# Kernel tuning notes

Measured on AMD Instinct MI355X. Metric: run time of the kernel, lower is better.

## Reference

```python
import jax, jax.numpy as jnp
import numpy as np

B, T, D = 8, 2048, 128        # batch, time, input_dim
C, CD = 8192, 128             # codebook_size, codebook_dim
COMMIT_W = 1.0                # commitment_weight
IN2Q_W = 0.25                 # input_to_quantize_commit_loss_weight
EPS = 1e-12


def setup_inputs() -> dict:
    key = jax.random.key(0)
    k = jax.random.split(key, 4)
    z = jax.random.normal(k[0], (B, T, D), jnp.float32)
    frozen_codebook = jax.random.normal(k[1], (C, CD), jnp.float32) * CD ** -0.5
    conv_v = jax.random.normal(k[2], (D, CD), jnp.float32) * CD ** -0.5  # weight-norm direction (1x1 conv weight squeezed)
    conv_g = jnp.linalg.norm(conv_v, axis=1)                             # weight-norm gain (torch init: g = ||v||)
    conv_b = jnp.zeros((D,), jnp.float32)
    return {"z": z, "frozen_codebook": frozen_codebook, "conv_v": conv_v,
            "conv_g": conv_g, "conv_b": conv_b}


def _implicit_codebook(fc, v, g, b):
    # weight-normed 1x1 conv == linear: w = g * v / ||v||_row ; out = fc @ w.T + b
    w = g[:, None] * v / jnp.linalg.norm(v, axis=1, keepdims=True)
    return fc @ w.T + b  # (C, D)


def _rotate_to(src, tgt):
    # rotation trick (Fifty et al.): Householder-style rotation, grads flow only through src
    sg = jax.lax.stop_gradient
    norm_src = jnp.linalg.norm(src, axis=-1, keepdims=True)
    norm_tgt = jnp.linalg.norm(tgt, axis=-1, keepdims=True)
    u = sg(src / jnp.maximum(norm_src, EPS))
    q = sg(tgt / jnp.maximum(norm_tgt, EPS))
    w = u + q
    w = sg(w / jnp.maximum(jnp.linalg.norm(w, axis=-1, keepdims=True), EPS))
    e = src
    rotated = (e
               - 2.0 * jnp.sum(e * w, -1, keepdims=True) * w
               + 2.0 * jnp.sum(e * u, -1, keepdims=True) * q)
    scale = sg(norm_tgt / jnp.maximum(norm_src, EPS))
    return rotated * scale


def reference(z, frozen_codebook, conv_v, conv_g, conv_b):
    sg = jax.lax.stop_gradient
    cb = _implicit_codebook(frozen_codebook, conv_v, conv_g, conv_b)  # (C, D)
    # squared euclidean distances -> same argmin as torch.cdist (p=2)
    d2 = (jnp.sum(z * z, -1, keepdims=True)
          - 2.0 * jnp.einsum('btd,cd->btc', z, cb)
          + jnp.sum(cb * cb, -1))                                     # (B, T, C)
    indices = jnp.argmin(d2, axis=-1)                                 # (B, T)
    z_q = cb[indices]                                                 # (B, T, D)
    commit = (jnp.mean((sg(z) - z_q) ** 2)
              + IN2Q_W * jnp.mean((z - sg(z_q)) ** 2))
    z_q = _rotate_to(z, z_q)
    return z_q, indices, commit * COMMIT_W
```

## Files before the change

kernel.cpp:

```cpp
#include <hip/hip_runtime.h>
#include <math.h>

#define NROWS 16384
#define DIM 128
#define NCODE 8192
#define EPSF 1e-12f

typedef float f32x4 __attribute__((ext_vector_type(4)));
typedef __bf16 bf16x8 __attribute__((ext_vector_type(8)));
typedef unsigned short u16x8 __attribute__((ext_vector_type(8)));

#define WS_NEED_BYTES 31571968ull

#define KT 12
#define TILEA 4096
#define TILEB 8192

__device__ __forceinline__ float wave_sum(float x) {
#pragma unroll
  for (int off = 32; off > 0; off >>= 1) x += __shfl_xor(x, off, 64);
  return x;
}

__device__ __forceinline__ unsigned short f2bf(float x) {
  union { float f; unsigned int u; } v;
  v.f = x;
  unsigned int r = v.u + 0x7fffu + ((v.u >> 16) & 1u);
  return (unsigned short)(r >> 16);
}
__device__ __forceinline__ float bf2f(unsigned short h) {
  union { float f; unsigned int u; } v;
  v.u = ((unsigned int)h) << 16;
  return v.f;
}

__device__ __forceinline__ void gload_lds16(const unsigned short* g,
                                            unsigned short* l) {
  __builtin_amdgcn_global_load_lds(
      (const __attribute__((address_space(1))) void*)g,
      (__attribute__((address_space(3))) void*)l, 16, 0, 0);
}

__global__ void wprep_kernel(const float* __restrict__ v,
                             const float* __restrict__ g,
                             float* __restrict__ Wt) {
  const int d = blockIdx.x;
  const int lane = threadIdx.x;
  const float v0 = v[d * DIM + lane], v1 = v[d * DIM + lane + 64];
  const float ss = wave_sum(fmaf(v0, v0, v1 * v1));
  const float sc = g[d] / sqrtf(ss);
  Wt[lane * DIM + d] = v0 * sc;
  Wt[(lane + 64) * DIM + d] = v1 * sc;
}

__global__ __launch_bounds__(256, 2) void codebook_kernel(
    const float* __restrict__ fc, const float* __restrict__ Wt,
    const float* __restrict__ bias, float* __restrict__ cb,
    float* __restrict__ cnorm2, unsigned short* __restrict__ cbcat) {
  __shared__ float Ws[DIM][DIM];
  const int tid = threadIdx.x;
  for (int i = tid; i < 4096; i += 256)
    *(float4*)&Ws[0][i << 2] = *(const float4*)&Wt[i << 2];
  __syncthreads();

  const int lane = tid & 63, wid = tid >> 6;
  const int c0 = blockIdx.x * 16 + wid * 4;
  const float b0 = bias[lane], b1 = bias[lane + 64];

  for (int cc = 0; cc < 4; ++cc) {
    const int c = __builtin_amdgcn_readfirstlane(c0 + cc);
    float a0 = 0.f, a1 = 0.f;
    for (int k = 0; k < DIM; k += 4) {
      const float4 f4 = *(const float4*)&fc[c * DIM + k];
      a0 = fmaf(f4.x, Ws[k][lane], a0);
      a1 = fmaf(f4.x, Ws[k][lane + 64], a1);
      a0 = fmaf(f4.y, Ws[k + 1][lane], a0);
      a1 = fmaf(f4.y, Ws[k + 1][lane + 64], a1);
      a0 = fmaf(f4.z, Ws[k + 2][lane], a0);
      a1 = fmaf(f4.z, Ws[k + 2][lane + 64], a1);
      a0 = fmaf(f4.w, Ws[k + 3][lane], a0);
      a1 = fmaf(f4.w, Ws[k + 3][lane + 64], a1);
    }
    const float o0 = a0 + b0, o1 = a1 + b1;
    cb[c * DIM + lane] = o0;
    cb[c * DIM + lane + 64] = o1;
    const float ss = wave_sum(fmaf(o0, o0, o1 * o1));
    if (lane == 0) cnorm2[c] = ss;

    if (cbcat != nullptr) {
      const int ct = c >> 8, r = c & 255;
      const unsigned int swz = ((r >> 1) & 3) << 3;
      unsigned short* base = cbcat + (size_t)ct * (KT * TILEB);
#pragma unroll
      for (int h = 0; h < 2; ++h) {
        const int d = lane + 64 * h;
        const float val = h ? o1 : o0;
        const unsigned short hi = f2bf(val);
        const unsigned short lo = f2bf(val - bf2f(hi));
        const int ktl = d >> 5;
        const int off = (r << 5) + ((d & 31) ^ swz);
        base[ktl * TILEB + off] = hi;
        base[(4 + ktl) * TILEB + off] = lo;
        base[(8 + ktl) * TILEB + off] = hi;
      }
    }
  }
}

__global__ __launch_bounds__(256) void zprep_kernel(
    const float* __restrict__ z, unsigned short* __restrict__ zcat) {
  const int id = blockIdx.x * 256 + threadIdx.x;
  const int row = id / 48, s = id - row * 48;
  const int kt = s >> 2, s4 = s & 3;
  const int seg = kt >> 2;
  const int d0 = ((kt & 3) << 5) + (s4 << 3);
  const int r = row & 127, rt = row >> 7;
  const int slotsw = s4 ^ ((r >> 1) & 3);

  const float* zp = &z[(size_t)row * DIM + d0];
  u16x8 out;
#pragma unroll
  for (int i = 0; i < 8; ++i) {
    const float x = zp[i];
    unsigned short b = f2bf(x);
    if (seg == 2) b = f2bf(x - bf2f(b));
    out[i] = b;
  }
  *(u16x8*)&zcat[(size_t)(rt * KT + kt) * TILEA + (r << 5) + (slotsw << 3)] =
      out;
}

__global__ __launch_bounds__(512, 4) void mfma_argmin_kernel(
    const unsigned short* __restrict__ zcat,
    const unsigned short* __restrict__ cbcat,
    const float* __restrict__ cnorm2, float* __restrict__ pval,
    int* __restrict__ pidx) {
  __shared__ __align__(16) unsigned short S[TILEA + TILEB];

  const int xcd = blockIdx.x & 7, idx = blockIdx.x >> 3;
  const int rt = xcd * 16 + (idx & 15);
  const int ct = idx >> 4;

  const int tid = threadIdx.x;
  const int lane = tid & 63, wid = tid >> 6;
  const int wr = wid >> 2, wc = wid & 3;
  const int l15 = lane & 15, lg = lane >> 4;
  const int tid8 = tid * 8;

  const unsigned short* Ag = zcat + (size_t)rt * (KT * TILEA);
  const unsigned short* Bg = cbcat + (size_t)ct * (KT * TILEB);

  f32x4 acc[4][4];
#pragma unroll
  for (int mi = 0; mi < 4; ++mi)
#pragma unroll
    for (int ni = 0; ni < 4; ++ni) acc[mi][ni] = f32x4{0.f, 0.f, 0.f, 0.f};

  int aoff[4], boff[4];
#pragma unroll
  for (int i = 0; i < 4; ++i) {
    const int ra = wr * 64 + i * 16 + l15;
    aoff[i] = (ra << 5) + ((lg ^ ((ra >> 1) & 3)) << 3);
    const int rc = wc * 64 + i * 16 + l15;
    boff[i] = TILEA + (rc << 5) + ((lg ^ ((rc >> 1) & 3)) << 3);
  }

  for (int kt = 0; kt < KT; ++kt) {
    __syncthreads();
    gload_lds16(Ag + kt * TILEA + tid8, &S[tid8]);
    gload_lds16(Bg + kt * TILEB + tid8, &S[TILEA + tid8]);
    gload_lds16(Bg + kt * TILEB + 4096 + tid8, &S[TILEA + 4096 + tid8]);
    __syncthreads();

    bf16x8 af[4], bfr[4];
#pragma unroll
    for (int i = 0; i < 4; ++i) af[i] = *(const bf16x8*)&S[aoff[i]];
#pragma unroll
    for (int i = 0; i < 4; ++i) bfr[i] = *(const bf16x8*)&S[boff[i]];
#pragma unroll
    for (int mi = 0; mi < 4; ++mi)
#pragma unroll
      for (int ni = 0; ni < 4; ++ni)
        acc[mi][ni] = __builtin_amdgcn_mfma_f32_16x16x32_bf16(
            af[mi], bfr[ni], acc[mi][ni], 0, 0, 0);
  }
  __syncthreads();

  float* exv = (float*)&S[0];
  int* exi = (int*)&S[2048];

  float cn[4];
#pragma unroll
  for (int ni = 0; ni < 4; ++ni)
    cn[ni] = cnorm2[ct * 256 + wc * 64 + ni * 16 + l15];

#pragma unroll
  for (int mi = 0; mi < 4; ++mi) {
#pragma unroll
    for (int rg = 0; rg < 4; ++rg) {
      float bv = 3.4e38f;
      int bi = 0;
#pragma unroll
      for (int ni = 0; ni < 4; ++ni) {
        const float d = fmaf(-2.f, acc[mi][ni][rg], cn[ni]);
        if (d < bv) { bv = d; bi = ct * 256 + wc * 64 + ni * 16 + l15; }
      }
#pragma unroll
      for (int off = 1; off < 16; off <<= 1) {
        const float ov = __shfl_xor(bv, off, 64);
        const int oi = __shfl_xor(bi, off, 64);
        if (ov < bv || (ov == bv && oi < bi)) { bv = ov; bi = oi; }
      }
      if (l15 == 0) {
        const int rloc = wr * 64 + mi * 16 + (lg << 2) + rg;
        exv[wc * 128 + rloc] = bv;
        exi[wc * 128 + rloc] = bi;
      }
    }
  }
  __syncthreads();
  if (tid < 128) {
    float bv = exv[tid];
    int bi = exi[tid];
#pragma unroll
    for (int w = 1; w < 4; ++w) {
      const float v = exv[w * 128 + tid];
      if (v < bv) { bv = v; bi = exi[w * 128 + tid]; }
    }
    const int row = rt * 128 + tid;
    pval[(size_t)ct * NROWS + row] = bv;
    pidx[(size_t)ct * NROWS + row] = bi;
  }
}

__global__ __launch_bounds__(256, 1) void argmin_kernel(
    const float* __restrict__ z, const float* __restrict__ cb,
    const float* __restrict__ cnorm2, float* __restrict__ pval,
    int* __restrict__ pidx) {
  __shared__ float zs[128][DIM];
  __shared__ float cs[128][DIM];

  const int tid = threadIdx.x;
  const int rb = blockIdx.x >> 1;
  const int ch = blockIdx.x & 1;
  const int row0 = rb * 128;
  const int code0 = ch * (NCODE / 2);

  for (int i = tid; i < 128 * 32; i += 256) {
    const int r = i >> 5, f = i & 31;
    *(float4*)&zs[r][f << 2] = *(const float4*)&z[(row0 + r) * DIM + (f << 2)];
  }

  const int tx = tid & 15, ty = tid >> 4;
  const int sw = tx & 7;

  float best[8];
  int besti[8];
#pragma unroll
  for (int r = 0; r < 8; ++r) { best[r] = 3.4e38f; besti[r] = 0; }

  for (int cc = 0; cc < NCODE / 2; cc += 128) {
    __syncthreads();
    for (int i = tid; i < 128 * 32; i += 256) {
      const int r = i >> 5, f = i & 31;
      const int fg = f ^ (r & 7);
      *(float4*)&cs[r][f << 2] =
          *(const float4*)&cb[(code0 + cc + r) * DIM + (fg << 2)];
    }
    __syncthreads();

    float acc[8][8];
#pragma unroll
    for (int r = 0; r < 8; ++r)
#pragma unroll
      for (int j = 0; j < 8; ++j) acc[r][j] = 0.f;

    for (int k = 0; k < DIM; k += 4) {
      const int f = k >> 2;
      float4 zr[8], cr[8];
#pragma unroll
      for (int r = 0; r < 8; ++r) zr[r] = *(const float4*)&zs[ty + 16 * r][k];
      const int col = ((f ^ sw) << 2);
#pragma unroll
      for (int j = 0; j < 8; ++j) cr[j] = *(const float4*)&cs[tx + 16 * j][col];
#pragma unroll
      for (int r = 0; r < 8; ++r)
#pragma unroll
        for (int j = 0; j < 8; ++j) {
          acc[r][j] = fmaf(zr[r].x, cr[j].x, acc[r][j]);
          acc[r][j] = fmaf(zr[r].y, cr[j].y, acc[r][j]);
          acc[r][j] = fmaf(zr[r].z, cr[j].z, acc[r][j]);
          acc[r][j] = fmaf(zr[r].w, cr[j].w, acc[r][j]);
        }
    }

#pragma unroll
    for (int j = 0; j < 8; ++j) {
      const int code = code0 + cc + tx + 16 * j;
      const float cnv = cnorm2[code];
#pragma unroll
      for (int r = 0; r < 8; ++r) {
        const float s = fmaf(-2.f, acc[r][j], cnv);
        if (s < best[r]) { best[r] = s; besti[r] = code; }
      }
    }
  }

#pragma unroll
  for (int off = 1; off < 16; off <<= 1) {
#pragma unroll
    for (int r = 0; r < 8; ++r) {
      const float ov = __shfl_xor(best[r], off, 64);
      const int oi = __shfl_xor(besti[r], off, 64);
      if (ov < best[r] || (ov == best[r] && oi < besti[r])) {
        best[r] = ov;
        besti[r] = oi;
      }
    }
  }
  if (tx == 0) {
#pragma unroll
    for (int r = 0; r < 8; ++r) {
      const int row = row0 + ty + 16 * r;
      pval[(size_t)ch * NROWS + row] = best[r];
      pidx[(size_t)ch * NROWS + row] = besti[r];
    }
  }
}

__global__ __launch_bounds__(256) void rotate_kernel(
    const float* __restrict__ z, const float* __restrict__ cb,
    const float* __restrict__ pval, const int* __restrict__ pidx, int ntiles,
    float* __restrict__ out_zq, float* __restrict__ out_idx,
    float* __restrict__ partials) {
  const int tid = threadIdx.x;
  const int wid = tid >> 6, lane = tid & 63;
  const int row = blockIdx.x * 4 + wid;

  float bv = 3.4e38f;
  int bi = 0x7fffffff;
  if (lane < ntiles) {
    bv = pval[(size_t)lane * NROWS + row];
    bi = pidx[(size_t)lane * NROWS + row];
  }
#pragma unroll
  for (int off = 32; off > 0; off >>= 1) {
    const float ov = __shfl_xor(bv, off, 64);
    const int oi = __shfl_xor(bi, off, 64);
    if (ov < bv || (ov == bv && oi < bi)) { bv = ov; bi = oi; }
  }
  const int ci = bi;

  const float z0 = z[row * DIM + lane], z1 = z[row * DIM + lane + 64];
  const float c0 = cb[ci * DIM + lane], c1 = cb[ci * DIM + lane + 64];

  const float ns2 = wave_sum(fmaf(z0, z0, z1 * z1));
  const float nt2 = wave_sum(fmaf(c0, c0, c1 * c1));
  const float ns = sqrtf(ns2), nt = sqrtf(nt2);
  const float dns = fmaxf(ns, EPSF), dnt = fmaxf(nt, EPSF);
  const float u0 = z0 / dns, u1 = z1 / dns;
  const float q0 = c0 / dnt, q1 = c1 / dnt;
  float w0 = u0 + q0, w1 = u1 + q1;
  const float nw = sqrtf(wave_sum(fmaf(w0, w0, w1 * w1)));
  const float dnw = fmaxf(nw, EPSF);
  w0 /= dnw;
  w1 /= dnw;
  const float ew = wave_sum(fmaf(z0, w0, z1 * w1));
  const float eu = wave_sum(fmaf(z0, u0, z1 * u1));
  const float sc = nt / dns;
  const float o0 = (z0 - 2.f * ew * w0 + 2.f * eu * q0) * sc;
  const float o1 = (z1 - 2.f * ew * w1 + 2.f * eu * q1) * sc;
  out_zq[row * DIM + lane] = o0;
  out_zq[row * DIM + lane + 64] = o1;
  if (lane == 0) out_idx[row] = (float)ci;

  const float d0 = z0 - c0, d1 = z1 - c1;
  const float rsum = wave_sum(fmaf(d0, d0, d1 * d1));
  __shared__ float pr[4];
  if (lane == 0) pr[wid] = rsum;
  __syncthreads();
  if (tid == 0) partials[blockIdx.x] = (pr[0] + pr[1]) + (pr[2] + pr[3]);
}

__global__ void finalize_kernel(const float* __restrict__ partials,
                                float* __restrict__ out_commit) {
  __shared__ float red[256];
  const int tid = threadIdx.x;
  float s = 0.f;
  for (int i = tid; i < 4096; i += 256) s += partials[i];
  red[tid] = s;
  __syncthreads();
  for (int off = 128; off > 0; off >>= 1) {
    if (tid < off) red[tid] += red[tid + off];
    __syncthreads();
  }
  if (tid == 0) out_commit[0] = red[0] * (1.25f / ((float)NROWS * (float)DIM));
}

extern "C" void kernel_launch(void* const* d_in, const int* in_sizes, int n_in,
                              void* d_out, int out_size, void* d_ws,
                              size_t ws_size, hipStream_t stream) {
  const float* z = (const float*)d_in[0];
  const float* fc = (const float*)d_in[1];
  const float* conv_v = (const float*)d_in[2];
  const float* conv_g = (const float*)d_in[3];
  const float* conv_b = (const float*)d_in[4];
  float* out = (float*)d_out;

  float* ws = (float*)d_ws;
  float* cb = ws;
  float* cnorm2 = ws + 1048576;
  float* Wt = ws + 1056768;

  if (ws_size >= WS_NEED_BYTES) {
    unsigned short* zcat = (unsigned short*)(ws + 1073152);
    unsigned short* cbcat = (unsigned short*)(ws + 4218880);
    float* pval = ws + 5791744;
    int* pidx = (int*)(ws + 6840320);
    float* partials = ws + 7888896;

    wprep_kernel<<<DIM, 64, 0, stream>>>(conv_v, conv_g, Wt);
    codebook_kernel<<<NCODE / 16, 256, 0, stream>>>(fc, Wt, conv_b, cb, cnorm2,
                                                    cbcat);
    zprep_kernel<<<NROWS * 48 / 256, 256, 0, stream>>>(z, zcat);
    mfma_argmin_kernel<<<4096, 512, 0, stream>>>(zcat, cbcat, cnorm2, pval,
                                                 pidx);
    rotate_kernel<<<NROWS / 4, 256, 0, stream>>>(z, cb, pval, pidx, 32, out,
                                                 out + 2097152, partials);
    finalize_kernel<<<1, 256, 0, stream>>>(partials, out + 2113536);
  } else {
    float* pval = ws + 1073152;
    int* pidx = (int*)(ws + 1105920);
    float* partials = ws + 1138688;

    wprep_kernel<<<DIM, 64, 0, stream>>>(conv_v, conv_g, Wt);
    codebook_kernel<<<NCODE / 16, 256, 0, stream>>>(fc, Wt, conv_b, cb, cnorm2,
                                                    nullptr);
    argmin_kernel<<<256, 256, 0, stream>>>(z, cb, cnorm2, pval, pidx);
    rotate_kernel<<<NROWS / 4, 256, 0, stream>>>(z, cb, pval, pidx, 2, out,
                                                 out + 2097152, partials);
    finalize_kernel<<<1, 256, 0, stream>>>(partials, out + 2113536);
  }
}
```

Before: 212.8 us.

## Double-buffer LDS tiles to overlap global loads with MFMA compute

Splits the shared-memory staging buffer into two halves and prefetches the next K tile with direct global-to-LDS loads while MFMAs consume the current one. Manual vmcnt waits and raw s_barrier calls replace the two __syncthreads per iteration, and the K loop is fully unrolled. This is meant to hide global load latency in the distance GEMM. In exchange LDS use doubles to about 48KB per block, which may limit occupancy under launch_bounds(512,4).

```diff
diff --git a/kernel.cpp b/kernel.cpp
--- a/kernel.cpp
+++ b/kernel.cpp
@@ -15,6 +15,7 @@
 #define KT 12
 #define TILEA 4096
 #define TILEB 8192
+#define CHUNK (TILEA + TILEB)
 
 __device__ __forceinline__ float wave_sum(float x) {
 #pragma unroll
@@ -95,13 +96,13 @@
       for (int h = 0; h < 2; ++h) {
         const int d = lane + 64 * h;
         const float val = h ? o1 : o0;
-        const unsigned short hi = f2bf(val);
-        const unsigned short lo = f2bf(val - bf2f(hi));
+        const unsigned short hiv = f2bf(val);
+        const unsigned short lov = f2bf(val - bf2f(hiv));
         const int ktl = d >> 5;
         const int off = (r << 5) + ((d & 31) ^ swz);
-        base[ktl * TILEB + off] = hi;
-        base[(4 + ktl) * TILEB + off] = lo;
-        base[(8 + ktl) * TILEB + off] = hi;
+        base[ktl * TILEB + off] = hiv;
+        base[(4 + ktl) * TILEB + off] = lov;
+        base[(8 + ktl) * TILEB + off] = hiv;
       }
     }
   }
@@ -135,7 +136,7 @@
     const unsigned short* __restrict__ cbcat,
     const float* __restrict__ cnorm2, float* __restrict__ pval,
     int* __restrict__ pidx) {
-  __shared__ __align__(16) unsigned short S[TILEA + TILEB];
+  __shared__ __align__(16) unsigned short S[2 * CHUNK];
 
   const int xcd = blockIdx.x & 7, idx = blockIdx.x >> 3;
   const int rt = xcd * 16 + (idx & 15);
@@ -150,6 +151,14 @@
   const unsigned short* Ag = zcat + (size_t)rt * (KT * TILEA);
   const unsigned short* Bg = cbcat + (size_t)ct * (KT * TILEB);
 
+#define STAGE(ktile, buf)                                                  \
+  do {                                                                     \
+    gload_lds16(Ag + (ktile)*TILEA + tid8, &S[(buf)*CHUNK + tid8]);        \
+    gload_lds16(Bg + (ktile)*TILEB + tid8, &S[(buf)*CHUNK + TILEA + tid8]); \
+    gload_lds16(Bg + (ktile)*TILEB + 4096 + tid8,                          \
+                &S[(buf)*CHUNK + TILEA + 4096 + tid8]);                    \
+  } while (0)
+
   f32x4 acc[4][4];
 #pragma unroll
   for (int mi = 0; mi < 4; ++mi)
@@ -165,25 +174,38 @@
     boff[i] = TILEA + (rc << 5) + ((lg ^ ((rc >> 1) & 3)) << 3);
   }
 
+  STAGE(0, 0);
+
+#pragma unroll
   for (int kt = 0; kt < KT; ++kt) {
-    __syncthreads();
-    gload_lds16(Ag + kt * TILEA + tid8, &S[tid8]);
-    gload_lds16(Bg + kt * TILEB + tid8, &S[TILEA + tid8]);
-    gload_lds16(Bg + kt * TILEB + 4096 + tid8, &S[TILEA + 4096 + tid8]);
-    __syncthreads();
+    const int cur = kt & 1;
+    if (kt + 1 < KT) {
+      STAGE(kt + 1, cur ^ 1);
+      asm volatile("s_waitcnt vmcnt(3)" ::: "memory");
+    } else {
+      asm volatile("s_waitcnt vmcnt(0)" ::: "memory");
+    }
+    __builtin_amdgcn_sched_barrier(0);
+    __builtin_amdgcn_s_barrier();
+    __builtin_amdgcn_sched_barrier(0);
 
     bf16x8 af[4], bfr[4];
 #pragma unroll
-    for (int i = 0; i < 4; ++i) af[i] = *(const bf16x8*)&S[aoff[i]];
-#pragma unroll
-    for (int i = 0; i < 4; ++i) bfr[i] = *(const bf16x8*)&S[boff[i]];
+    for (int i = 0; i < 4; ++i) af[i] = *(const bf16x8*)&S[cur * CHUNK + aoff[i]];
+#pragma unroll
+    for (int i = 0; i < 4; ++i) bfr[i] = *(const bf16x8*)&S[cur * CHUNK + boff[i]];
 #pragma unroll
     for (int mi = 0; mi < 4; ++mi)
 #pragma unroll
       for (int ni = 0; ni < 4; ++ni)
         acc[mi][ni] = __builtin_amdgcn_mfma_f32_16x16x32_bf16(
             af[mi], bfr[ni], acc[mi][ni], 0, 0, 0);
-  }
+
+    __builtin_amdgcn_sched_barrier(0);
+    __builtin_amdgcn_s_barrier();
+    __builtin_amdgcn_sched_barrier(0);
+  }
+#undef STAGE
   __syncthreads();
 
   float* exv = (float*)&S[0];
```

New measurement: 217.7 us. 1.02x slower.
